# Performance work log

Hardware: AMD Instinct MI355X
Metric: run time of the kernel (lower is better)

## Reference

```python
import jax, jax.numpy as jnp
import numpy as np

B, S, D, H = 4, 2048, 1024, 16
HD = D // H
MASKED_BIAS = -10000.0

def setup_inputs() -> dict:
    key = jax.random.key(0)
    ks = jax.random.split(key, 10)
    s = 0.02
    return {
        "hidden_states": jax.random.normal(ks[0], (B, S, D), dtype=jnp.float32),
        "Wq": jax.random.normal(ks[1], (D, D), dtype=jnp.float32) * s,
        "bq": jax.random.normal(ks[2], (D,), dtype=jnp.float32) * s,
        "Wk": jax.random.normal(ks[3], (D, D), dtype=jnp.float32) * s,
        "bk": jax.random.normal(ks[4], (D,), dtype=jnp.float32) * s,
        "Wv": jax.random.normal(ks[5], (D, D), dtype=jnp.float32) * s,
        "bv": jax.random.normal(ks[6], (D,), dtype=jnp.float32) * s,
        "Wo": jax.random.normal(ks[7], (D, D), dtype=jnp.float32) * s,
        "bo": jax.random.normal(ks[8], (D,), dtype=jnp.float32) * s,
        "comp": jnp.zeros((D,), dtype=jnp.float32),
    }

def reference(hidden_states, Wq, bq, Wk, bk, Wv, bv, Wo, bo, comp):
    x = hidden_states
    # torch Linear: y = x @ W.T + b
    q = (x @ Wq.T + bq).reshape(B, S, H, HD).transpose(0, 2, 1, 3)  # [B,H,S,hd]
    k = (x @ Wk.T + bk).reshape(B, S, H, HD).transpose(0, 2, 1, 3)
    v = (x @ Wv.T + bv).reshape(B, S, H, HD).transpose(0, 2, 1, 3)
    scores = jnp.einsum('bhqd,bhkd->bhqk', q, k) / jnp.sqrt(jnp.asarray(HD, dtype=q.dtype))
    causal = jnp.tril(jnp.ones((S, S), dtype=bool))  # [S,S]
    scores = jnp.where(causal[None, None], scores, jnp.asarray(MASKED_BIAS, dtype=scores.dtype))
    attn = jax.nn.softmax(scores, axis=-1)  # dropout p=0 (eval)
    out = jnp.einsum('bhqk,bhkd->bhqd', attn, v)  # [B,H,S,hd]
    out = out.transpose(0, 2, 1, 3).reshape(B, S, D)
    out = out @ Wo.T + bo
    out = out + comp[None, None, :]
    return out
```

## Files before the change

kernel.cpp:

```cpp
#include <hip/hip_runtime.h>
#include <hip/hip_bf16.h>

#define NB 4
#define NS 2048
#define ND 1024
#define NH 16
#define NHD 64
#define NM (NB*NS)

typedef __bf16 bf16_t;
typedef bf16_t bf8  __attribute__((ext_vector_type(8)));
typedef bf16_t bf4v __attribute__((ext_vector_type(4)));
typedef float  f4   __attribute__((ext_vector_type(4)));

#define GLDS16(g, l) __builtin_amdgcn_global_load_lds( \
    (const __attribute__((address_space(1))) void*)(g), \
    (__attribute__((address_space(3))) void*)(l), 16, 0, 0)

__global__ __launch_bounds__(256) void cvt_all(const float* __restrict__ x,
                                               const float* __restrict__ wq,
                                               const float* __restrict__ wk,
                                               const float* __restrict__ wv,
                                               const float* __restrict__ wo,
                                               bf16_t* __restrict__ Xb,
                                               bf16_t* __restrict__ Wqkv,
                                               bf16_t* __restrict__ Wob) {
    const int i = blockIdx.x * 256 + threadIdx.x;
    const float* src;
    bf16_t* dst;
    int off;
    if (i < 2097152) {
        src = x; dst = Xb; off = i;
    } else {
        const int j = i - 2097152;
        const int w = j >> 18;
        off = j & 262143;
        src = (w == 0 ? wq : w == 1 ? wk : w == 2 ? wv : wo);
        dst = (w == 3 ? Wob : Wqkv + ((size_t)w << 20));
    }
    const float4 v = ((const float4*)src)[off];
    bf4v o;
    o[0] = (bf16_t)v.x; o[1] = (bf16_t)v.y; o[2] = (bf16_t)v.z; o[3] = (bf16_t)v.w;
    ((bf4v*)dst)[off] = o;
}

__global__ __launch_bounds__(256) void gemm_qkv(const bf16_t* __restrict__ A,
                                                const bf16_t* __restrict__ Bw,
                                                const float* __restrict__ bq,
                                                const float* __restrict__ bk,
                                                const float* __restrict__ bv,
                                                bf16_t* __restrict__ Qh,
                                                bf16_t* __restrict__ Kh,
                                                bf16_t* __restrict__ Vh) {
    __shared__ __align__(16) bf16_t As[128 * 32];
    __shared__ __align__(16) bf16_t Bs[128 * 32];
    const int t = threadIdx.x;
    const int wave = t >> 6, lane = t & 63, ln = lane & 15, quad = lane >> 4;
    const int wm = (wave >> 1) * 64, wn = (wave & 1) * 64;
    const int m0 = blockIdx.y * 128, n0 = blockIdx.x * 128;
    const int K = 1024;

    f4 acc[4][4];
    const f4 z = {0.f, 0.f, 0.f, 0.f};
#pragma unroll
    for (int i = 0; i < 4; ++i)
#pragma unroll
        for (int j = 0; j < 4; ++j) acc[i][j] = z;

    const int srow = wave * 16 + (lane >> 2);
    const int scol = (lane & 3) * 8;
    const bf16_t* Ag0 = A  + (size_t)(m0 + srow) * K + scol;
    const bf16_t* Ag1 = A  + (size_t)(m0 + srow + 64) * K + scol;
    const bf16_t* Bg0 = Bw + (size_t)(n0 + srow) * K + scol;
    const bf16_t* Bg1 = Bw + (size_t)(n0 + srow + 64) * K + scol;
    bf16_t* Al0 = &As[srow * 32 + scol];
    bf16_t* Al1 = &As[(srow + 64) * 32 + scol];
    bf16_t* Bl0 = &Bs[srow * 32 + scol];
    bf16_t* Bl1 = &Bs[(srow + 64) * 32 + scol];

    for (int k0 = 0; k0 < K; k0 += 32) {
        __syncthreads();
        GLDS16(Ag0 + k0, Al0);
        GLDS16(Ag1 + k0, Al1);
        GLDS16(Bg0 + k0, Bl0);
        GLDS16(Bg1 + k0, Bl1);
        __syncthreads();
        bf8 af[4], bfr[4];
#pragma unroll
        for (int mt = 0; mt < 4; ++mt) af[mt]  = *(const bf8*)(&As[(wm + mt * 16 + ln) * 32 + quad * 8]);
#pragma unroll
        for (int nt = 0; nt < 4; ++nt) bfr[nt] = *(const bf8*)(&Bs[(wn + nt * 16 + ln) * 32 + quad * 8]);
#pragma unroll
        for (int mt = 0; mt < 4; ++mt)
#pragma unroll
            for (int nt = 0; nt < 4; ++nt)
                acc[mt][nt] = __builtin_amdgcn_mfma_f32_16x16x32_bf16(af[mt], bfr[nt], acc[mt][nt], 0, 0, 0);
    }

#pragma unroll
    for (int nt = 0; nt < 4; ++nt) {
        const int gn = n0 + wn + nt * 16 + ln;
        const int sec = gn >> 10, nn = gn & 1023;
        const int h = nn >> 6, d = nn & 63;
        const float bias = (sec == 0 ? bq[nn] : (sec == 1 ? bk[nn] : bv[nn]));
        bf16_t* dstBase = (sec == 0 ? Qh : (sec == 1 ? Kh : Vh));
#pragma unroll
        for (int mt = 0; mt < 4; ++mt) {
#pragma unroll
            for (int r = 0; r < 4; ++r) {
                const int gm = m0 + wm + mt * 16 + quad * 4 + r;
                const int b = gm >> 11, s = gm & 2047;
                dstBase[((size_t)(b * NH + h) * NS + s) * NHD + d] = (bf16_t)(acc[mt][nt][r] + bias);
            }
        }
    }
}

__global__ __launch_bounds__(256) void attn_kernel(const bf16_t* __restrict__ Q,
                                                   const bf16_t* __restrict__ K,
                                                   const bf16_t* __restrict__ V,
                                                   bf16_t* __restrict__ O) {
    __shared__ __align__(16) bf16_t Ks[64 * 72];
    __shared__ __align__(16) bf16_t Vt[64 * 72];
    __shared__ __align__(16) bf16_t Ps[4][16 * 72];
    const int L = blockIdx.x;
    const int mm = L >> 3;
    const int h  = ((mm >> 5) << 3) | (L & 7);
    const int qt = 31 - (mm & 31);
    const int q0 = qt * 64;
    const int jmax = qt;
    const size_t head_off = (size_t)h * NS * NHD;
    const int t = threadIdx.x;
    const int wave = t >> 6, lane = t & 63, ln = lane & 15, quad = lane >> 4;

    const bf16_t* Qrow = Q + head_off + (size_t)(q0 + wave * 16 + ln) * NHD;
    bf8 qf0 = *(const bf8*)(Qrow + quad * 8);
    bf8 qf1 = *(const bf8*)(Qrow + 32 + quad * 8);
#pragma unroll
    for (int e = 0; e < 8; ++e) {
        qf0[e] = (bf16_t)((float)qf0[e] * 0.125f);
        qf1[e] = (bf16_t)((float)qf1[e] * 0.125f);
    }

    const bf16_t* Kg = K + head_off;
    const bf16_t* Vg = V + head_off;
    const int krow0 = t >> 3, kcol = (t & 7) * 8;

    uint4 kr0 = *(const uint4*)(Kg + (size_t)krow0 * NHD + kcol);
    uint4 kr1 = *(const uint4*)(Kg + (size_t)(krow0 + 32) * NHD + kcol);
    bf8  vr0 = *(const bf8*)(Vg + (size_t)lane * NHD + wave * 8);
    bf8  vr1 = *(const bf8*)(Vg + (size_t)lane * NHD + (wave + 4) * 8);
    *(uint4*)(&Ks[krow0 * 72 + kcol])        = kr0;
    *(uint4*)(&Ks[(krow0 + 32) * 72 + kcol]) = kr1;
#pragma unroll
    for (int e = 0; e < 8; ++e) {
        Vt[(wave * 8 + e) * 72 + lane]       = vr0[e];
        Vt[((wave + 4) * 8 + e) * 72 + lane] = vr1[e];
    }
    __syncthreads();

    f4 o[4];
    const f4 z = {0.f, 0.f, 0.f, 0.f};
#pragma unroll
    for (int i = 0; i < 4; ++i) o[i] = z;
    float ls[4] = {0.f, 0.f, 0.f, 0.f};

    bf16_t* Pw = &Ps[wave][0];
    const int pswz = (ln >> 2) << 3;

#pragma unroll 1
    for (int j = 0; j <= jmax; ++j) {
        if (j < jmax) {
            const size_t nb = (size_t)(j + 1) * 64;
            kr0 = *(const uint4*)(Kg + (nb + krow0) * NHD + kcol);
            kr1 = *(const uint4*)(Kg + (nb + krow0 + 32) * NHD + kcol);
            vr0 = *(const bf8*)(Vg + (nb + lane) * NHD + wave * 8);
            vr1 = *(const bf8*)(Vg + (nb + lane) * NHD + (wave + 4) * 8);
        }

        f4 s[4];
        __builtin_amdgcn_s_setprio(1);
#pragma unroll
        for (int nt = 0; nt < 4; ++nt) {
            const bf8 kf0 = *(const bf8*)(&Ks[(nt * 16 + ln) * 72 + quad * 8]);
            const bf8 kf1 = *(const bf8*)(&Ks[(nt * 16 + ln) * 72 + 32 + quad * 8]);
            s[nt] = z;
            s[nt] = __builtin_amdgcn_mfma_f32_16x16x32_bf16(qf0, kf0, s[nt], 0, 0, 0);
            s[nt] = __builtin_amdgcn_mfma_f32_16x16x32_bf16(qf1, kf1, s[nt], 0, 0, 0);
        }
        __builtin_amdgcn_s_setprio(0);

        if (j == jmax) {
            const int kv0 = j * 64;
            const int rowg = q0 + wave * 16 + quad * 4;
#pragma unroll
            for (int nt = 0; nt < 4; ++nt) {
                const int col = kv0 + nt * 16 + ln;
#pragma unroll
                for (int r = 0; r < 4; ++r)
                    if (col > rowg + r) s[nt][r] = -1e30f;
            }
        }

#pragma unroll
        for (int nt = 0; nt < 4; ++nt)
#pragma unroll
            for (int r = 0; r < 4; ++r) {
                const float p = __expf(s[nt][r]);
                s[nt][r] = p;
                ls[r] += p;
            }

#pragma unroll
        for (int nt = 0; nt < 4; ++nt)
#pragma unroll
            for (int r = 0; r < 4; ++r)
                Pw[(quad * 4 + r) * 72 + ((nt * 16 + ln) ^ (quad << 3))] = (bf16_t)s[nt][r];
        asm volatile("s_waitcnt lgkmcnt(0)" ::: "memory");
        __builtin_amdgcn_sched_barrier(0);
        const bf8 p0 = *(const bf8*)(&Pw[ln * 72 + ((quad * 8) ^ pswz)]);
        const bf8 p1 = *(const bf8*)(&Pw[ln * 72 + 32 + ((quad * 8) ^ pswz)]);

        __builtin_amdgcn_s_setprio(1);
#pragma unroll
        for (int dt = 0; dt < 4; ++dt) {
            const bf8 v0 = *(const bf8*)(&Vt[(dt * 16 + ln) * 72 + quad * 8]);
            const bf8 v1 = *(const bf8*)(&Vt[(dt * 16 + ln) * 72 + 32 + quad * 8]);
            o[dt] = __builtin_amdgcn_mfma_f32_16x16x32_bf16(p0, v0, o[dt], 0, 0, 0);
            o[dt] = __builtin_amdgcn_mfma_f32_16x16x32_bf16(p1, v1, o[dt], 0, 0, 0);
        }
        __builtin_amdgcn_s_setprio(0);

        if (j < jmax) {
            __syncthreads();
            *(uint4*)(&Ks[krow0 * 72 + kcol])        = kr0;
            *(uint4*)(&Ks[(krow0 + 32) * 72 + kcol]) = kr1;
#pragma unroll
            for (int e = 0; e < 8; ++e) {
                Vt[(wave * 8 + e) * 72 + lane]       = vr0[e];
                Vt[((wave + 4) * 8 + e) * 72 + lane] = vr1[e];
            }
            __syncthreads();
        }
    }

#pragma unroll
    for (int off = 1; off < 16; off <<= 1)
#pragma unroll
        for (int r = 0; r < 4; ++r) ls[r] += __shfl_xor(ls[r], off);

    const int b = h >> 4, hh = h & 15;
#pragma unroll
    for (int r = 0; r < 4; ++r) {
        const float inv = 1.f / ls[r];
        const int gs = q0 + wave * 16 + quad * 4 + r;
#pragma unroll
        for (int dt = 0; dt < 4; ++dt)
            O[((size_t)(b * NS + gs)) * ND + hh * NHD + dt * 16 + ln] = (bf16_t)(o[dt][r] * inv);
    }
}

__global__ __launch_bounds__(256) void gemm_proj(const bf16_t* __restrict__ A,
                                                 const bf16_t* __restrict__ Bw,
                                                 const float* __restrict__ bo,
                                                 const float* __restrict__ comp,
                                                 float* __restrict__ out) {
    __shared__ __align__(16) bf16_t As[128 * 32];
    __shared__ __align__(16) bf16_t Bs[128 * 32];
    const int t = threadIdx.x;
    const int wave = t >> 6, lane = t & 63, ln = lane & 15, quad = lane >> 4;
    const int wm = (wave >> 1) * 64, wn = (wave & 1) * 64;
    const int m0 = blockIdx.y * 128, n0 = blockIdx.x * 128;
    const int K = 1024;

    f4 acc[4][4];
    const f4 z = {0.f, 0.f, 0.f, 0.f};
#pragma unroll
    for (int i = 0; i < 4; ++i)
#pragma unroll
        for (int j = 0; j < 4; ++j) acc[i][j] = z;

    const int srow = wave * 16 + (lane >> 2);
    const int scol = (lane & 3) * 8;
    const bf16_t* Ag0 = A  + (size_t)(m0 + srow) * K + scol;
    const bf16_t* Ag1 = A  + (size_t)(m0 + srow + 64) * K + scol;
    const bf16_t* Bg0 = Bw + (size_t)(n0 + srow) * K + scol;
    const bf16_t* Bg1 = Bw + (size_t)(n0 + srow + 64) * K + scol;
    bf16_t* Al0 = &As[srow * 32 + scol];
    bf16_t* Al1 = &As[(srow + 64) * 32 + scol];
    bf16_t* Bl0 = &Bs[srow * 32 + scol];
    bf16_t* Bl1 = &Bs[(srow + 64) * 32 + scol];

    for (int k0 = 0; k0 < K; k0 += 32) {
        __syncthreads();
        GLDS16(Ag0 + k0, Al0);
        GLDS16(Ag1 + k0, Al1);
        GLDS16(Bg0 + k0, Bl0);
        GLDS16(Bg1 + k0, Bl1);
        __syncthreads();
        bf8 af[4], bfr[4];
#pragma unroll
        for (int mt = 0; mt < 4; ++mt) af[mt]  = *(const bf8*)(&As[(wm + mt * 16 + ln) * 32 + quad * 8]);
#pragma unroll
        for (int nt = 0; nt < 4; ++nt) bfr[nt] = *(const bf8*)(&Bs[(wn + nt * 16 + ln) * 32 + quad * 8]);
#pragma unroll
        for (int mt = 0; mt < 4; ++mt)
#pragma unroll
            for (int nt = 0; nt < 4; ++nt)
                acc[mt][nt] = __builtin_amdgcn_mfma_f32_16x16x32_bf16(af[mt], bfr[nt], acc[mt][nt], 0, 0, 0);
    }

#pragma unroll
    for (int nt = 0; nt < 4; ++nt) {
        const int gn = n0 + wn + nt * 16 + ln;
        const float bias = bo[gn] + comp[gn];
#pragma unroll
        for (int mt = 0; mt < 4; ++mt) {
#pragma unroll
            for (int r = 0; r < 4; ++r) {
                const int gm = m0 + wm + mt * 16 + quad * 4 + r;
                out[(size_t)gm * ND + gn] = acc[mt][nt][r] + bias;
            }
        }
    }
}

extern "C" void kernel_launch(void* const* d_in, const int* in_sizes, int n_in,
                              void* d_out, int out_size, void* d_ws, size_t ws_size,
                              hipStream_t stream) {
    const float* x    = (const float*)d_in[0];
    const float* Wq   = (const float*)d_in[1];
    const float* bq   = (const float*)d_in[2];
    const float* Wk   = (const float*)d_in[3];
    const float* bk   = (const float*)d_in[4];
    const float* Wv   = (const float*)d_in[5];
    const float* bv   = (const float*)d_in[6];
    const float* Wo   = (const float*)d_in[7];
    const float* bo   = (const float*)d_in[8];
    const float* comp = (const float*)d_in[9];
    float* out = (float*)d_out;

    char* w = (char*)d_ws;
    bf16_t* Xb   = (bf16_t*)(w);
    bf16_t* Wqkv = (bf16_t*)(w + 16777216);
    bf16_t* Wob  = (bf16_t*)(w + 23068672);
    bf16_t* Qh   = (bf16_t*)(w + 25165824);
    bf16_t* Kh   = (bf16_t*)(w + 41943040);
    bf16_t* Vh   = (bf16_t*)(w + 58720256);
    bf16_t* AOb  = (bf16_t*)(w + 75497472);

    cvt_all<<<12288, 256, 0, stream>>>(x, Wq, Wk, Wv, Wo, Xb, Wqkv, Wob);
    gemm_qkv<<<dim3(3072 / 128, NM / 128), 256, 0, stream>>>(Xb, Wqkv, bq, bk, bv, Qh, Kh, Vh);
    attn_kernel<<<2048, 256, 0, stream>>>(Qh, Kh, Vh, AOb);
    gemm_proj<<<dim3(1024 / 128, NM / 128), 256, 0, stream>>>(AOb, Wob, bo, comp, out);
}
```

Before: 289.5 us.

## Process two query tiles per attention block with double-buffered K/V

Each attention block now covers 128 query rows as two 64-row strips that share every K/V tile staged in LDS. This halves the global K/V traffic and the staging work per query row, and the grid shrinks to 1024 blocks. K/V tiles are double-buffered in LDS, so each iteration needs one barrier instead of two. The cost is more registers (two accumulator sets and two Q fragments), more LDS per block, and coarser, less even work per block under the causal mask.

```diff
diff --git a/kernel.cpp b/kernel.cpp
--- a/kernel.cpp
+++ b/kernel.cpp
@@ -120,26 +120,32 @@
                                                    const bf16_t* __restrict__ K,
                                                    const bf16_t* __restrict__ V,
                                                    bf16_t* __restrict__ O) {
-    __shared__ __align__(16) bf16_t Ks[64 * 72];
-    __shared__ __align__(16) bf16_t Vt[64 * 72];
+    __shared__ __align__(16) bf16_t Ks[2][64 * 72];
+    __shared__ __align__(16) bf16_t Vt[2][64 * 72];
     __shared__ __align__(16) bf16_t Ps[4][16 * 72];
     const int L = blockIdx.x;
     const int mm = L >> 3;
-    const int h  = ((mm >> 5) << 3) | (L & 7);
-    const int qt = 31 - (mm & 31);
-    const int q0 = qt * 64;
-    const int jmax = qt;
+    const int h  = ((mm >> 4) << 3) | (L & 7);
+    const int qt = 15 - (mm & 15);
+    const int q0 = qt * 128;
+    const int jmax  = 2 * qt + 1;
+    const int j0max = 2 * qt;
     const size_t head_off = (size_t)h * NS * NHD;
     const int t = threadIdx.x;
     const int wave = t >> 6, lane = t & 63, ln = lane & 15, quad = lane >> 4;
 
-    const bf16_t* Qrow = Q + head_off + (size_t)(q0 + wave * 16 + ln) * NHD;
-    bf8 qf0 = *(const bf8*)(Qrow + quad * 8);
-    bf8 qf1 = *(const bf8*)(Qrow + 32 + quad * 8);
+    const bf16_t* Qrow0 = Q + head_off + (size_t)(q0 + wave * 16 + ln) * NHD;
+    const bf16_t* Qrow1 = Qrow0 + (size_t)64 * NHD;
+    bf8 qa0 = *(const bf8*)(Qrow0 + quad * 8);
+    bf8 qa1 = *(const bf8*)(Qrow0 + 32 + quad * 8);
+    bf8 qb0 = *(const bf8*)(Qrow1 + quad * 8);
+    bf8 qb1 = *(const bf8*)(Qrow1 + 32 + quad * 8);
 #pragma unroll
     for (int e = 0; e < 8; ++e) {
-        qf0[e] = (bf16_t)((float)qf0[e] * 0.125f);
-        qf1[e] = (bf16_t)((float)qf1[e] * 0.125f);
+        qa0[e] = (bf16_t)((float)qa0[e] * 0.125f);
+        qa1[e] = (bf16_t)((float)qa1[e] * 0.125f);
+        qb0[e] = (bf16_t)((float)qb0[e] * 0.125f);
+        qb1[e] = (bf16_t)((float)qb1[e] * 0.125f);
     }
 
     const bf16_t* Kg = K + head_off;
@@ -150,26 +156,79 @@
     uint4 kr1 = *(const uint4*)(Kg + (size_t)(krow0 + 32) * NHD + kcol);
     bf8  vr0 = *(const bf8*)(Vg + (size_t)lane * NHD + wave * 8);
     bf8  vr1 = *(const bf8*)(Vg + (size_t)lane * NHD + (wave + 4) * 8);
-    *(uint4*)(&Ks[krow0 * 72 + kcol])        = kr0;
-    *(uint4*)(&Ks[(krow0 + 32) * 72 + kcol]) = kr1;
+    *(uint4*)(&Ks[0][krow0 * 72 + kcol])        = kr0;
+    *(uint4*)(&Ks[0][(krow0 + 32) * 72 + kcol]) = kr1;
 #pragma unroll
     for (int e = 0; e < 8; ++e) {
-        Vt[(wave * 8 + e) * 72 + lane]       = vr0[e];
-        Vt[((wave + 4) * 8 + e) * 72 + lane] = vr1[e];
+        Vt[0][(wave * 8 + e) * 72 + lane]       = vr0[e];
+        Vt[0][((wave + 4) * 8 + e) * 72 + lane] = vr1[e];
     }
     __syncthreads();
 
-    f4 o[4];
+    f4 o0[4], o1[4];
     const f4 z = {0.f, 0.f, 0.f, 0.f};
 #pragma unroll
-    for (int i = 0; i < 4; ++i) o[i] = z;
-    float ls[4] = {0.f, 0.f, 0.f, 0.f};
+    for (int i = 0; i < 4; ++i) { o0[i] = z; o1[i] = z; }
+    float ls0[4] = {0.f, 0.f, 0.f, 0.f};
+    float ls1[4] = {0.f, 0.f, 0.f, 0.f};
 
     bf16_t* Pw = &Ps[wave][0];
     const int pswz = (ln >> 2) << 3;
 
+#define DO_STRIP(QF0, QF1, OA, LS, DIAG, ROWB)                                        \
+    {                                                                                 \
+        f4 s[4];                                                                      \
+        __builtin_amdgcn_s_setprio(1);                                                \
+        _Pragma("unroll")                                                             \
+        for (int nt = 0; nt < 4; ++nt) {                                              \
+            const bf8 kf0 = *(const bf8*)(&KsB[(nt * 16 + ln) * 72 + quad * 8]);      \
+            const bf8 kf1 = *(const bf8*)(&KsB[(nt * 16 + ln) * 72 + 32 + quad * 8]); \
+            s[nt] = z;                                                                \
+            s[nt] = __builtin_amdgcn_mfma_f32_16x16x32_bf16(QF0, kf0, s[nt], 0, 0, 0);\
+            s[nt] = __builtin_amdgcn_mfma_f32_16x16x32_bf16(QF1, kf1, s[nt], 0, 0, 0);\
+        }                                                                             \
+        __builtin_amdgcn_s_setprio(0);                                                \
+        if (DIAG) {                                                                   \
+            const int rowg = (ROWB) + quad * 4;                                       \
+            _Pragma("unroll")                                                         \
+            for (int nt = 0; nt < 4; ++nt) {                                          \
+                const int col = kv0 + nt * 16 + ln;                                   \
+                _Pragma("unroll")                                                     \
+                for (int r = 0; r < 4; ++r)                                           \
+                    if (col > rowg + r) s[nt][r] = -1e30f;                            \
+            }                                                                         \
+        }                                                                             \
+        _Pragma("unroll")                                                             \
+        for (int nt = 0; nt < 4; ++nt)                                                \
+            _Pragma("unroll")                                                         \
+            for (int r = 0; r < 4; ++r) {                                             \
+                const float p = __expf(s[nt][r]);                                     \
+                s[nt][r] = p;                                                         \
+                LS[r] += p;                                                           \
+            }                                                                         \
+        _Pragma("unroll")                                                             \
+        for (int nt = 0; nt < 4; ++nt)                                                \
+            _Pragma("unroll")                                                         \
+            for (int r = 0; r < 4; ++r)                                               \
+                Pw[(quad * 4 + r) * 72 + ((nt * 16 + ln) ^ (quad << 3))] =            \
+                    (bf16_t)s[nt][r];                                                 \
+        const bf8 p0 = *(const bf8*)(&Pw[ln * 72 + ((quad * 8) ^ pswz)]);             \
+        const bf8 p1 = *(const bf8*)(&Pw[ln * 72 + 32 + ((quad * 8) ^ pswz)]);        \
+        __builtin_amdgcn_s_setprio(1);                                                \
+        _Pragma("unroll")                                                             \
+        for (int dt = 0; dt < 4; ++dt) {                                              \
+            const bf8 v0 = *(const bf8*)(&VtB[(dt * 16 + ln) * 72 + quad * 8]);       \
+            const bf8 v1 = *(const bf8*)(&VtB[(dt * 16 + ln) * 72 + 32 + quad * 8]);  \
+            OA[dt] = __builtin_amdgcn_mfma_f32_16x16x32_bf16(p0, v0, OA[dt], 0, 0, 0);\
+            OA[dt] = __builtin_amdgcn_mfma_f32_16x16x32_bf16(p1, v1, OA[dt], 0, 0, 0);\
+        }                                                                             \
+        __builtin_amdgcn_s_setprio(0);                                                \
+    }
+
 #pragma unroll 1
     for (int j = 0; j <= jmax; ++j) {
+        const bf16_t* KsB = &Ks[j & 1][0];
+        const bf16_t* VtB = &Vt[j & 1][0];
         if (j < jmax) {
             const size_t nb = (size_t)(j + 1) * 64;
             kr0 = *(const uint4*)(Kg + (nb + krow0) * NHD + kcol);
@@ -177,86 +236,46 @@
             vr0 = *(const bf8*)(Vg + (nb + lane) * NHD + wave * 8);
             vr1 = *(const bf8*)(Vg + (nb + lane) * NHD + (wave + 4) * 8);
         }
-
-        f4 s[4];
-        __builtin_amdgcn_s_setprio(1);
-#pragma unroll
-        for (int nt = 0; nt < 4; ++nt) {
-            const bf8 kf0 = *(const bf8*)(&Ks[(nt * 16 + ln) * 72 + quad * 8]);
-            const bf8 kf1 = *(const bf8*)(&Ks[(nt * 16 + ln) * 72 + 32 + quad * 8]);
-            s[nt] = z;
-            s[nt] = __builtin_amdgcn_mfma_f32_16x16x32_bf16(qf0, kf0, s[nt], 0, 0, 0);
-            s[nt] = __builtin_amdgcn_mfma_f32_16x16x32_bf16(qf1, kf1, s[nt], 0, 0, 0);
-        }
-        __builtin_amdgcn_s_setprio(0);
-
-        if (j == jmax) {
-            const int kv0 = j * 64;
-            const int rowg = q0 + wave * 16 + quad * 4;
-#pragma unroll
-            for (int nt = 0; nt < 4; ++nt) {
-                const int col = kv0 + nt * 16 + ln;
-#pragma unroll
-                for (int r = 0; r < 4; ++r)
-                    if (col > rowg + r) s[nt][r] = -1e30f;
+        const int kv0 = j * 64;
+
+        if (j <= j0max) DO_STRIP(qa0, qa1, o0, ls0, j == j0max, q0 + wave * 16);
+        DO_STRIP(qb0, qb1, o1, ls1, j == jmax, q0 + 64 + wave * 16);
+
+        if (j < jmax) {
+            bf16_t* KsN = &Ks[(j + 1) & 1][0];
+            bf16_t* VtN = &Vt[(j + 1) & 1][0];
+            *(uint4*)(&KsN[krow0 * 72 + kcol])        = kr0;
+            *(uint4*)(&KsN[(krow0 + 32) * 72 + kcol]) = kr1;
+#pragma unroll
+            for (int e = 0; e < 8; ++e) {
+                VtN[(wave * 8 + e) * 72 + lane]       = vr0[e];
+                VtN[((wave + 4) * 8 + e) * 72 + lane] = vr1[e];
             }
         }
-
-#pragma unroll
-        for (int nt = 0; nt < 4; ++nt)
-#pragma unroll
-            for (int r = 0; r < 4; ++r) {
-                const float p = __expf(s[nt][r]);
-                s[nt][r] = p;
-                ls[r] += p;
-            }
-
-#pragma unroll
-        for (int nt = 0; nt < 4; ++nt)
-#pragma unroll
-            for (int r = 0; r < 4; ++r)
-                Pw[(quad * 4 + r) * 72 + ((nt * 16 + ln) ^ (quad << 3))] = (bf16_t)s[nt][r];
-        asm volatile("s_waitcnt lgkmcnt(0)" ::: "memory");
-        __builtin_amdgcn_sched_barrier(0);
-        const bf8 p0 = *(const bf8*)(&Pw[ln * 72 + ((quad * 8) ^ pswz)]);
-        const bf8 p1 = *(const bf8*)(&Pw[ln * 72 + 32 + ((quad * 8) ^ pswz)]);
-
-        __builtin_amdgcn_s_setprio(1);
+        __syncthreads();
+    }
+#undef DO_STRIP
+
+#pragma unroll
+    for (int off = 1; off < 16; off <<= 1)
+#pragma unroll
+        for (int r = 0; r < 4; ++r) {
+            ls0[r] += __shfl_xor(ls0[r], off);
+            ls1[r] += __shfl_xor(ls1[r], off);
+        }
+
+    const int b = h >> 4, hh = h & 15;
+#pragma unroll
+    for (int r = 0; r < 4; ++r) {
+        const float inv0 = 1.f / ls0[r];
+        const float inv1 = 1.f / ls1[r];
+        const int gs0 = q0 + wave * 16 + quad * 4 + r;
+        const int gs1 = gs0 + 64;
 #pragma unroll
         for (int dt = 0; dt < 4; ++dt) {
-            const bf8 v0 = *(const bf8*)(&Vt[(dt * 16 + ln) * 72 + quad * 8]);
-            const bf8 v1 = *(const bf8*)(&Vt[(dt * 16 + ln) * 72 + 32 + quad * 8]);
-            o[dt] = __builtin_amdgcn_mfma_f32_16x16x32_bf16(p0, v0, o[dt], 0, 0, 0);
-            o[dt] = __builtin_amdgcn_mfma_f32_16x16x32_bf16(p1, v1, o[dt], 0, 0, 0);
-        }
-        __builtin_amdgcn_s_setprio(0);
-
-        if (j < jmax) {
-            __syncthreads();
-            *(uint4*)(&Ks[krow0 * 72 + kcol])        = kr0;
-            *(uint4*)(&Ks[(krow0 + 32) * 72 + kcol]) = kr1;
-#pragma unroll
-            for (int e = 0; e < 8; ++e) {
-                Vt[(wave * 8 + e) * 72 + lane]       = vr0[e];
-                Vt[((wave + 4) * 8 + e) * 72 + lane] = vr1[e];
-            }
-            __syncthreads();
-        }
-    }
-
-#pragma unroll
-    for (int off = 1; off < 16; off <<= 1)
-#pragma unroll
-        for (int r = 0; r < 4; ++r) ls[r] += __shfl_xor(ls[r], off);
-
-    const int b = h >> 4, hh = h & 15;
-#pragma unroll
-    for (int r = 0; r < 4; ++r) {
-        const float inv = 1.f / ls[r];
-        const int gs = q0 + wave * 16 + quad * 4 + r;
-#pragma unroll
-        for (int dt = 0; dt < 4; ++dt)
-            O[((size_t)(b * NS + gs)) * ND + hh * NHD + dt * 16 + ln] = (bf16_t)(o[dt][r] * inv);
+            O[((size_t)(b * NS + gs0)) * ND + hh * NHD + dt * 16 + ln] = (bf16_t)(o0[dt][r] * inv0);
+            O[((size_t)(b * NS + gs1)) * ND + hh * NHD + dt * 16 + ln] = (bf16_t)(o1[dt][r] * inv1);
+        }
     }
 }
 
@@ -351,6 +370,6 @@
 
     cvt_all<<<12288, 256, 0, stream>>>(x, Wq, Wk, Wv, Wo, Xb, Wqkv, Wob);
     gemm_qkv<<<dim3(3072 / 128, NM / 128), 256, 0, stream>>>(Xb, Wqkv, bq, bk, bv, Qh, Kh, Vh);
-    attn_kernel<<<2048, 256, 0, stream>>>(Qh, Kh, Vh, AOb);
+    attn_kernel<<<1024, 256, 0, stream>>>(Qh, Kh, Vh, AOb);
     gemm_proj<<<dim3(1024 / 128, NM / 128), 256, 0, stream>>>(AOb, Wob, bo, comp, out);
 }
```

New measurement: 315.8 us. 9.1% more time.
